# Optimization experiments

Hardware: AMD Instinct MI355X
Metric: run time of the kernel (lower is better)

## Reference

```python
import jax, jax.numpy as jnp
import numpy as np

NHID = 512
NCLS = 250
CHUNK = 200  # words per class (equal class_chunks), vocab = NCLS*CHUNK = 50000
N = 2048     # flattened tokens (batch*seq after masking)


def setup_inputs() -> dict:
    key = jax.random.key(0)
    k1, k2, k3, k4, k5 = jax.random.split(key, 5)
    r = 0.1  # init_weights uniform range
    x = jax.random.normal(k1, (N, NHID), dtype=jnp.float32)
    cls_idx = jax.random.randint(k2, (N,), 0, NCLS, dtype=jnp.int64)
    Wc = jax.random.uniform(k3, (NCLS, NHID), jnp.float32, -r, r)   # cls_decoder.weight
    bc = jnp.zeros((NCLS,), jnp.float32)                             # cls_decoder.bias
    Ww = jax.random.uniform(k4, (NCLS, CHUNK, NHID), jnp.float32, -r, r)  # stacked words_decoders weights
    bw = jnp.zeros((NCLS, CHUNK), jnp.float32)                       # stacked words_decoders biases
    return {"x": x, "Wc": Wc, "bc": bc, "Ww": Ww, "bw": bw, "cls_idx": cls_idx}


def reference(x, Wc, bc, Ww, bw, cls_idx):
    # Class logits for every token: cls_decoder(input)
    p_class = jnp.einsum('nh,ch->nc', x, Wc) + bc          # [N, NCLS]
    # Per-class word decoders: each token goes through the Linear of its class.
    # Equivalent to the dict-based index_select + per-class Linear in the
    # original forward (rows reordered per-token instead of grouped by class).
    Wg = Ww[cls_idx]                                       # [N, CHUNK, NHID] irregular gather
    bg = bw[cls_idx]                                       # [N, CHUNK]
    p_words = jnp.einsum('nkh,nh->nk', Wg, x) + bg         # [N, CHUNK]
    # Concatenate class and within-class logits into one array output.
    return jnp.concatenate([p_class, p_words], axis=1)     # [N, NCLS+CHUNK]
```

## Files before the change

kernel.cpp:

```cpp
#include <hip/hip_runtime.h>

#define NHID   512
#define NCLS   250
#define CHUNK  200
#define NTOK   2048
#define NOUT   450
#define NPAN   13
#define NWB    (NCLS * NPAN)
#define NCB    256
#define NBLK   (NWB + NCB)
#define NTHR   64
#define MAXTOK 64

typedef __attribute__((ext_vector_type(8))) short bf16x8;
typedef __attribute__((ext_vector_type(4))) float f32x4;

#define MFMA(a, b, c) __builtin_amdgcn_mfma_f32_16x16x32_bf16((a), (b), (c), 0, 0, 0)

#define BOFF(s) ((((s) >> 3) * 256) + (((s) & 7) * 32))

__device__ __forceinline__ unsigned hpack(unsigned a, unsigned b) {
    return __builtin_amdgcn_perm(a, b, 0x07060302u);
}

__device__ __forceinline__ void cvt8(float4 va, float4 vb, bf16x8& h, bf16x8& l) {
    unsigned u0 = __float_as_uint(va.x), u1 = __float_as_uint(va.y);
    unsigned u2 = __float_as_uint(va.z), u3 = __float_as_uint(va.w);
    unsigned u4 = __float_as_uint(vb.x), u5 = __float_as_uint(vb.y);
    unsigned u6 = __float_as_uint(vb.z), u7 = __float_as_uint(vb.w);
    union { unsigned w[4]; bf16x8 v; } H, L;
    H.w[0] = hpack(u1, u0); H.w[1] = hpack(u3, u2);
    H.w[2] = hpack(u5, u4); H.w[3] = hpack(u7, u6);
    float r0 = va.x - __uint_as_float(u0 & 0xffff0000u);
    float r1 = va.y - __uint_as_float(u1 & 0xffff0000u);
    float r2 = va.z - __uint_as_float(u2 & 0xffff0000u);
    float r3 = va.w - __uint_as_float(u3 & 0xffff0000u);
    float r4 = vb.x - __uint_as_float(u4 & 0xffff0000u);
    float r5 = vb.y - __uint_as_float(u5 & 0xffff0000u);
    float r6 = vb.z - __uint_as_float(u6 & 0xffff0000u);
    float r7 = vb.w - __uint_as_float(u7 & 0xffff0000u);
    L.w[0] = hpack(__float_as_uint(r1), __float_as_uint(r0));
    L.w[1] = hpack(__float_as_uint(r3), __float_as_uint(r2));
    L.w[2] = hpack(__float_as_uint(r5), __float_as_uint(r4));
    L.w[3] = hpack(__float_as_uint(r7), __float_as_uint(r6));
    h = H.v; l = L.v;
}

__device__ __forceinline__ void async16(const float* g, float* lds_base) {
    __builtin_amdgcn_global_load_lds(
        (const __attribute__((address_space(1))) unsigned*)g,
        (__attribute__((address_space(3))) unsigned*)lds_base, 16, 0, 0);
}

__device__ __forceinline__ void lds_fence_wave() {
    __builtin_amdgcn_wave_barrier();
    asm volatile("s_waitcnt lgkmcnt(0)" ::: "memory");
    __builtin_amdgcn_wave_barrier();
}

__global__ __launch_bounds__(NTHR)
void cbd_fused(const float* __restrict__ x,  const float* __restrict__ Wc,
               const float* __restrict__ bc, const float* __restrict__ Ww,
               const float* __restrict__ bw, const int* __restrict__ cls_idx,
               float* __restrict__ out)
{
    __shared__ float Bbuf[16 * 512];
    __shared__ int   toktmp[MAXTOK];

    const int bid  = blockIdx.x;
    const int lane = threadIdx.x;
    const int n    = lane & 15;
    const int q    = lane >> 4;

    if (bid < NCB) {
        const int mt = bid >> 1, hn = bid & 1;
        const float* ap = x + (size_t)(mt * 16 + n) * NHID + q * 8;
        #pragma unroll
        for (int g4 = 0; g4 < 2; ++g4) {
            const float* bp[4]; float bias[4]; int col[4]; bool rv[4];
            #pragma unroll
            for (int k = 0; k < 4; ++k) {
                int r = (hn * 8 + g4 * 4 + k) * 16 + n;
                rv[k] = r < NCLS;
                int rc = rv[k] ? r : NCLS - 1;
                bp[k]   = Wc + (size_t)rc * NHID + q * 8;
                bias[k] = bc[rc];
                col[k]  = rc;
            }
            f32x4 acc[4] = {{0,0,0,0},{0,0,0,0},{0,0,0,0},{0,0,0,0}};
            float4 qa[2][2], qb[2][8];
            #pragma unroll
            for (int j = 0; j < 2; ++j) {
                qa[j][0] = *(const float4*)(ap + j * 32);
                qa[j][1] = *(const float4*)(ap + j * 32 + 4);
                #pragma unroll
                for (int k = 0; k < 4; ++k) {
                    qb[j][2*k]   = *(const float4*)(bp[k] + j * 32);
                    qb[j][2*k+1] = *(const float4*)(bp[k] + j * 32 + 4);
                }
            }
            #pragma unroll 2
            for (int s = 0; s < 16; ++s) {
                const int b = s & 1;
                bf16x8 ah, al; cvt8(qa[b][0], qa[b][1], ah, al);
                #pragma unroll
                for (int k = 0; k < 4; ++k) {
                    bf16x8 bh, bl; cvt8(qb[b][2*k], qb[b][2*k+1], bh, bl);
                    acc[k] = MFMA(ah, bh, acc[k]);
                    acc[k] = MFMA(al, bh, acc[k]);
                    acc[k] = MFMA(ah, bl, acc[k]);
                }
                if (s + 2 < 16) {
                    qa[b][0] = *(const float4*)(ap + (s+2) * 32);
                    qa[b][1] = *(const float4*)(ap + (s+2) * 32 + 4);
                    #pragma unroll
                    for (int k = 0; k < 4; ++k) {
                        qb[b][2*k]   = *(const float4*)(bp[k] + (s+2) * 32);
                        qb[b][2*k+1] = *(const float4*)(bp[k] + (s+2) * 32 + 4);
                    }
                }
            }
            #pragma unroll
            for (int k = 0; k < 4; ++k)
                if (rv[k]) {
                    #pragma unroll
                    for (int i = 0; i < 4; ++i)
                        out[(size_t)(mt * 16 + q * 4 + i) * NOUT + col[k]]
                            = acc[k][i] + bias[k];
                }
        }
        return;
    }

    const int wb0 = bid - NCB;
    const int xcd  = wb0 & 7;
    const int slot = wb0 >> 3;
    const int base = (xcd < 2) ? xcd * 407 : 2 * 407 + (xcd - 2) * 406;
    const int wb   = base + slot;

    const int c = wb / NPAN;
    const int p = wb - c * NPAN;

    const int r  = p * 16 + n;
    const int rr = r < CHUNK ? r : CHUNK - 1;

    int myvals[32];
    #pragma unroll
    for (int it = 0; it < 8; ++it) {
        int4 v = *(const int4*)&cls_idx[it * 256 + lane * 4];
        myvals[it*4+0] = v.x; myvals[it*4+1] = v.y;
        myvals[it*4+2] = v.z; myvals[it*4+3] = v.w;
    }
    float bias = bw[c * CHUNK + rr];
    #pragma unroll
    for (int it = 0; it < 8; ++it)
        asm volatile("" :: "v"(myvals[it*4]), "v"(myvals[it*4+1]),
                           "v"(myvals[it*4+2]), "v"(myvals[it*4+3]));
    asm volatile("" :: "v"(bias));

    #pragma unroll
    for (int j = 0; j < 16; ++j) {
        int rj = p * 16 + j; if (rj > CHUNK - 1) rj = CHUNK - 1;
        const float* srow = Ww + ((size_t)c * CHUNK + rj) * NHID;
        const int lsw = (lane ^ (j & 7)) << 2;
        async16(srow + lsw,       &Bbuf[j * 512]);
        async16(srow + 256 + lsw, &Bbuf[j * 512 + 256]);
    }

    int cnt = 0;
    #pragma unroll
    for (int j = 0; j < 32; ++j) {
        int idx  = (j >> 2) * 256 + lane * 4 + (j & 3);
        bool hit = (myvals[j] == c);
        unsigned long long m = __ballot(hit);
        if (hit) {
            int pos = cnt + (int)__popcll(m & ((1ull << lane) - 1ull));
            if (pos < MAXTOK) toktmp[pos] = idx;
        }
        cnt += (int)__popcll(m);
    }
    if (cnt == 0) {
        asm volatile("s_waitcnt vmcnt(0)" ::: "memory");
        return;
    }
    const int cntc = cnt < MAXTOK ? cnt : MAXTOK;
    lds_fence_wave();

    const float* Bb0 = Bbuf + n * 512 + (((q * 8))     ^ ((n & 7) << 2));
    const float* Bb1 = Bbuf + n * 512 + (((q * 8) + 4) ^ ((n & 7) << 2));

    for (int sb = 0; sb < cntc; sb += 16) {
        int slotn = sb + n;
        int mytok = toktmp[slotn < cntc ? slotn : 0];
        int tkS[4]; bool msk[4];
        #pragma unroll
        for (int i = 0; i < 4; ++i) {
            int m = q * 4 + i;
            tkS[i] = __shfl(mytok, m);
            msk[i] = (sb + m) < cntc;
        }
        const float* apx = x + (size_t)mytok * NHID + q * 8;

        float4 pa[2][4];
        #pragma unroll
        for (int j = 0; j < 2; ++j)
            #pragma unroll
            for (int t = 0; t < 2; ++t) {
                pa[j][2*t]   = *(const float4*)(apx + (2*j + t) * 32);
                pa[j][2*t+1] = *(const float4*)(apx + (2*j + t) * 32 + 4);
            }
        asm volatile("s_waitcnt vmcnt(8)" ::: "memory");

        f32x4 acc = {0.f, 0.f, 0.f, 0.f};
        #pragma unroll
        for (int j = 0; j < 8; ++j) {
            const int b = j & 1;
            #pragma unroll
            for (int t = 0; t < 2; ++t) {
                const int s = 2 * j + t;
                bf16x8 ah, al, bh, bl;
                cvt8(pa[b][2*t], pa[b][2*t+1], ah, al);
                float4 b0 = *(const float4*)(Bb0 + BOFF(s));
                float4 b1 = *(const float4*)(Bb1 + BOFF(s));
                cvt8(b0, b1, bh, bl);
                acc = MFMA(ah, bh, acc);
                acc = MFMA(al, bh, acc);
                acc = MFMA(ah, bl, acc);
            }
            if (j + 2 < 8) {
                #pragma unroll
                for (int t = 0; t < 2; ++t) {
                    const int s = 2 * (j + 2) + t;
                    pa[b][2*t]   = *(const float4*)(apx + s * 32);
                    pa[b][2*t+1] = *(const float4*)(apx + s * 32 + 4);
                }
            }
        }

        if (r < CHUNK) {
            #pragma unroll
            for (int i = 0; i < 4; ++i)
                if (msk[i])
                    out[(size_t)tkS[i] * NOUT + NCLS + r] = acc[i] + bias;
        }
    }
}

extern "C" void kernel_launch(void* const* d_in, const int* in_sizes, int n_in,
                              void* d_out, int out_size, void* d_ws, size_t ws_size,
                              hipStream_t stream) {
    const float* x   = (const float*)d_in[0];
    const float* Wc  = (const float*)d_in[1];
    const float* bc  = (const float*)d_in[2];
    const float* Ww  = (const float*)d_in[3];
    const float* bw  = (const float*)d_in[4];
    const int*   cls = (const int*)d_in[5];
    float* out = (float*)d_out;
    hipLaunchKernelGGL(cbd_fused, dim3(NBLK), dim3(NTHR), 0, stream,
                       x, Wc, bc, Ww, bw, cls, out);
}
```

Baseline: 174.7 us.

## Add prefetch blocks that stream per-XCD Ww slices into L2 before compute

Adds 256 extra blocks at the front of the grid that read each XCD's assigned range of the word-decoder weights and discard the values. The intent is to warm that XCD's L2/MALL with the weights so the later word blocks hit in cache instead of waiting on HBM. The cost is extra blocks and an extra full read of the roughly 200MB Ww tensor. Because that tensor is far larger than the caches, much of the prefetched data may be evicted before the compute blocks use it. The scheme also assumes blocks are placed round-robin across XCDs by block index.

```diff
diff --git a/kernel.cpp b/kernel.cpp
--- a/kernel.cpp
+++ b/kernel.cpp
@@ -7,8 +7,9 @@
 #define NOUT   450
 #define NPAN   13
 #define NWB    (NCLS * NPAN)
+#define NSTR   256
 #define NCB    256
-#define NBLK   (NWB + NCB)
+#define NBLK   (NSTR + NCB + NWB)
 #define NTHR   64
 #define MAXTOK 64
 
@@ -72,8 +73,32 @@
     const int n    = lane & 15;
     const int q    = lane >> 4;
 
-    if (bid < NCB) {
-        const int mt = bid >> 1, hn = bid & 1;
+    if (bid < NSTR) {
+        const int sx = bid & 7;
+        const int sj = bid >> 3;
+        const int B0 = (sx < 2) ? sx * 407 : 2 * 407 + (sx - 2) * 406;
+        const int B1 = B0 + ((sx < 2) ? 407 : 406);
+        int c0 = B0 / NPAN;
+        int c1 = (B1 + NPAN - 1) / NPAN; if (c1 > NCLS) c1 = NCLS;
+        const f32x4* gb = (const f32x4*)(Ww + (size_t)c0 * CHUNK * NHID);
+        const int nf4 = (c1 - c0) * (CHUNK * NHID / 4);
+        const int stride = 2048 * 16;
+        for (int i = (sj * 64 + lane) * 16; i + 15 < nf4; i += stride) {
+            f32x4 a0 = gb[i+0],  a1 = gb[i+1],  a2 = gb[i+2],  a3 = gb[i+3];
+            f32x4 a4 = gb[i+4],  a5 = gb[i+5],  a6 = gb[i+6],  a7 = gb[i+7];
+            f32x4 a8 = gb[i+8],  a9 = gb[i+9],  aA = gb[i+10], aB = gb[i+11];
+            f32x4 aC = gb[i+12], aD = gb[i+13], aE = gb[i+14], aF = gb[i+15];
+            asm volatile("" :: "v"(a0),"v"(a1),"v"(a2),"v"(a3),
+                               "v"(a4),"v"(a5),"v"(a6),"v"(a7),
+                               "v"(a8),"v"(a9),"v"(aA),"v"(aB),
+                               "v"(aC),"v"(aD),"v"(aE),"v"(aF));
+        }
+        return;
+    }
+
+    if (bid < NSTR + NCB) {
+        const int pcb = bid - NSTR;
+        const int mt = pcb >> 1, hn = pcb & 1;
         const float* ap = x + (size_t)(mt * 16 + n) * NHID + q * 8;
         #pragma unroll
         for (int g4 = 0; g4 < 2; ++g4) {
@@ -132,7 +157,7 @@
         return;
     }
 
-    const int wb0 = bid - NCB;
+    const int wb0 = bid - (NSTR + NCB);
     const int xcd  = wb0 & 7;
     const int slot = wb0 >> 3;
     const int base = (xcd < 2) ? xcd * 407 : 2 * 407 + (xcd - 2) * 406;
```

New measurement: 176.2 us. No clear change (+0.9%).
